# Performance work log

Measured on AMD Instinct MI355X. Metric: run time of the kernel, lower is better.

Reference implementation:

```python
import jax, jax.numpy as jnp
import numpy as np

N_GAUSSIANS = 16
B, D = 32768, 64
LOG_2PI = float(np.log(2.0 * np.pi))


def setup_inputs() -> dict:
    key = jax.random.key(0)
    k1, k2, k3, k4 = jax.random.split(key, 4)
    means = jax.random.normal(k1, (B, N_GAUSSIANS * D), dtype=jnp.float32)
    # strictly positive diagonal variances in [0.5, 1.5)
    covs = jax.random.uniform(k2, (B, N_GAUSSIANS * D), dtype=jnp.float32) + 0.5
    # positive mixture weights (softmax-normalized, like a typical MDN head)
    weights = jax.nn.softmax(jax.random.normal(k3, (B, N_GAUSSIANS), dtype=jnp.float32), axis=-1)
    targets = jax.random.normal(k4, (B, D), dtype=jnp.float32)
    return {"means": means, "covs": covs, "weights": weights, "targets": targets}


def reference(means, covs, weights, targets):
    b = means.shape[0]
    mu = means.reshape(b, N_GAUSSIANS, -1)   # [B, K, D]
    var = covs.reshape(b, N_GAUSSIANS, -1)   # [B, K, D]
    t = targets[:, None, :]                  # [B, 1, D]
    d = mu.shape[-1]
    # analytic diagonal-Gaussian log-prob (same math as MultivariateNormal
    # with diag_embed covariance, without the Cholesky)
    quad = jnp.sum((t - mu) ** 2 / var, axis=-1)          # [B, K]
    logdet = jnp.sum(jnp.log(var), axis=-1)               # [B, K]
    log_probs = -0.5 * (d * LOG_2PI + logdet + quad)      # [B, K]
    log_probs = jnp.clip(log_probs, -100.0, 0.0)
    log_probs_weighted = log_probs + jnp.log(weights)
    total_log_likelihood = jax.nn.logsumexp(log_probs_weighted, axis=1)  # [B]
    return -1.0 * total_log_likelihood
```

## Files before the change

### kernel.cpp

```cpp
#include <hip/hip_runtime.h>
#include <math.h>

#define NG 16
#define DIM 64
#define LOG_2PI 1.8378770664093453f
#define RPW 4
#define WPB 4
#define ROWS_PER_BLOCK (RPW * WPB)

__global__ __launch_bounds__(256) void gmm_loss_kernel(
    const float* __restrict__ means,
    const float* __restrict__ covs,
    const float* __restrict__ weights,
    const float* __restrict__ targets,
    float* __restrict__ out, int B)
{
    const int lane = threadIdx.x & 63;
    const int wave = threadIdx.x >> 6;
    const int g  = lane >> 2;
    const int dq = lane & 3;
    const int fo = lane * 4;

    int b = blockIdx.x * ROWS_PER_BLOCK + wave * RPW;

    #pragma unroll 1
    for (int r = 0; r < RPW; ++r, ++b) {
        if (b >= B) break;

        const float4* m4 = (const float4*)(means + (size_t)b * (NG * DIM)) + fo;
        const float4* v4 = (const float4*)(covs  + (size_t)b * (NG * DIM)) + fo;
        const float4* t4 = (const float4*)(targets + (size_t)b * DIM) + dq * 4;

        const float  w  = weights[(size_t)b * NG + g];
        const float4 m0 = m4[0], m1 = m4[1], m2 = m4[2], m3 = m4[3];
        const float4 v0 = v4[0], v1 = v4[1], v2 = v4[2], v3 = v4[3];
        const float4 t0 = t4[0], t1 = t4[1], t2 = t4[2], t3 = t4[3];

        float p = 0.0f;
        float dx;
        dx = t0.x - m0.x; p += dx * dx * __builtin_amdgcn_rcpf(v0.x);
        dx = t0.y - m0.y; p += dx * dx * __builtin_amdgcn_rcpf(v0.y);
        dx = t0.z - m0.z; p += dx * dx * __builtin_amdgcn_rcpf(v0.z);
        dx = t0.w - m0.w; p += dx * dx * __builtin_amdgcn_rcpf(v0.w);
        p += __logf(v0.x * v0.y * v0.z * v0.w);

        dx = t1.x - m1.x; p += dx * dx * __builtin_amdgcn_rcpf(v1.x);
        dx = t1.y - m1.y; p += dx * dx * __builtin_amdgcn_rcpf(v1.y);
        dx = t1.z - m1.z; p += dx * dx * __builtin_amdgcn_rcpf(v1.z);
        dx = t1.w - m1.w; p += dx * dx * __builtin_amdgcn_rcpf(v1.w);
        p += __logf(v1.x * v1.y * v1.z * v1.w);

        dx = t2.x - m2.x; p += dx * dx * __builtin_amdgcn_rcpf(v2.x);
        dx = t2.y - m2.y; p += dx * dx * __builtin_amdgcn_rcpf(v2.y);
        dx = t2.z - m2.z; p += dx * dx * __builtin_amdgcn_rcpf(v2.z);
        dx = t2.w - m2.w; p += dx * dx * __builtin_amdgcn_rcpf(v2.w);
        p += __logf(v2.x * v2.y * v2.z * v2.w);

        dx = t3.x - m3.x; p += dx * dx * __builtin_amdgcn_rcpf(v3.x);
        dx = t3.y - m3.y; p += dx * dx * __builtin_amdgcn_rcpf(v3.y);
        dx = t3.z - m3.z; p += dx * dx * __builtin_amdgcn_rcpf(v3.z);
        dx = t3.w - m3.w; p += dx * dx * __builtin_amdgcn_rcpf(v3.w);
        p += __logf(v3.x * v3.y * v3.z * v3.w);

        p += __shfl_xor(p, 1);
        p += __shfl_xor(p, 2);

        float lp = -0.5f * (DIM * LOG_2PI + p);
        lp = fminf(fmaxf(lp, -100.0f), 0.0f);
        const float lw = lp + __logf(w);

        float M = lw;
        M = fmaxf(M, __shfl_xor(M, 4));
        M = fmaxf(M, __shfl_xor(M, 8));
        M = fmaxf(M, __shfl_xor(M, 16));
        M = fmaxf(M, __shfl_xor(M, 32));
        float e = __expf(lw - M);
        e += __shfl_xor(e, 4);
        e += __shfl_xor(e, 8);
        e += __shfl_xor(e, 16);
        e += __shfl_xor(e, 32);

        if (lane == 0) out[b] = -(M + __logf(e));
    }
}

extern "C" void kernel_launch(void* const* d_in, const int* in_sizes, int n_in,
                              void* d_out, int out_size, void* d_ws, size_t ws_size,
                              hipStream_t stream) {
    const float* means   = (const float*)d_in[0];
    const float* covs    = (const float*)d_in[1];
    const float* weights = (const float*)d_in[2];
    const float* targets = (const float*)d_in[3];
    float* out = (float*)d_out;

    const int B = in_sizes[0] / (NG * DIM);
    const int grid = (B + ROWS_PER_BLOCK - 1) / ROWS_PER_BLOCK;
    gmm_loss_kernel<<<grid, 256, 0, stream>>>(means, covs, weights, targets, out, B);
}
```

Before: 280.0 us.

## Double-buffer row loads with coalesced nontemporal reads and restructured reductions

Result: faster. 264.6 us (-5.5%).

```diff
diff --git a/kernel.cpp b/kernel.cpp
--- a/kernel.cpp
+++ b/kernel.cpp
@@ -8,6 +8,11 @@
 #define WPB 4
 #define ROWS_PER_BLOCK (RPW * WPB)
 
+typedef float f32x4 __attribute__((ext_vector_type(4)));
+
+
+#define NT(p) __builtin_nontemporal_load(p)
+
 __global__ __launch_bounds__(256) void gmm_loss_kernel(
     const float* __restrict__ means,
     const float* __restrict__ covs,
@@ -17,71 +22,99 @@
 {
     const int lane = threadIdx.x & 63;
     const int wave = threadIdx.x >> 6;
-    const int g  = lane >> 2;
-    const int dq = lane & 3;
-    const int fo = lane * 4;
+    const int G = lane >> 4;
+    const int c = lane & 15;
 
-    int b = blockIdx.x * ROWS_PER_BLOCK + wave * RPW;
+    const int b0 = blockIdx.x * ROWS_PER_BLOCK + wave * RPW;
 
-    #pragma unroll 1
-    for (int r = 0; r < RPW; ++r, ++b) {
-        if (b >= B) break;
+#define ISSUE(S, bb) {                                                        \
+        const int rb = (bb) < B ? (bb) : (B - 1);                             \
+        const f32x4* Mp = (const f32x4*)(means + (size_t)rb * (NG * DIM));    \
+        const f32x4* Vp = (const f32x4*)(covs  + (size_t)rb * (NG * DIM));    \
+        m0##S = NT(Mp + lane);       v0##S = NT(Vp + lane);                   \
+        m1##S = NT(Mp + lane + 64);  v1##S = NT(Vp + lane + 64);              \
+        m2##S = NT(Mp + lane + 128); v2##S = NT(Vp + lane + 128);             \
+        m3##S = NT(Mp + lane + 192); v3##S = NT(Vp + lane + 192);             \
+    }
 
-        const float4* m4 = (const float4*)(means + (size_t)b * (NG * DIM)) + fo;
-        const float4* v4 = (const float4*)(covs  + (size_t)b * (NG * DIM)) + fo;
-        const float4* t4 = (const float4*)(targets + (size_t)b * DIM) + dq * 4;
+#define COMPUTE(S, bb) {                                                      \
+        const int rb = (bb) < B ? (bb) : (B - 1);                             \
+        const f32x4 t = ((const f32x4*)(targets + (size_t)rb * DIM))[c];      \
+        const float* W = weights + (size_t)rb * NG;                           \
+        const float w0 = W[G];     const float w1 = W[G + 4];                 \
+        const float w2 = W[G + 8]; const float w3 = W[G + 12];                \
+        float dx, p0, p1, p2, p3;                                             \
+        dx = t.x - m0##S.x; p0  = dx * dx * __builtin_amdgcn_rcpf(v0##S.x);   \
+        dx = t.y - m0##S.y; p0 += dx * dx * __builtin_amdgcn_rcpf(v0##S.y);   \
+        dx = t.z - m0##S.z; p0 += dx * dx * __builtin_amdgcn_rcpf(v0##S.z);   \
+        dx = t.w - m0##S.w; p0 += dx * dx * __builtin_amdgcn_rcpf(v0##S.w);   \
+        p0 += __logf(v0##S.x * v0##S.y * v0##S.z * v0##S.w);                  \
+        dx = t.x - m1##S.x; p1  = dx * dx * __builtin_amdgcn_rcpf(v1##S.x);   \
+        dx = t.y - m1##S.y; p1 += dx * dx * __builtin_amdgcn_rcpf(v1##S.y);   \
+        dx = t.z - m1##S.z; p1 += dx * dx * __builtin_amdgcn_rcpf(v1##S.z);   \
+        dx = t.w - m1##S.w; p1 += dx * dx * __builtin_amdgcn_rcpf(v1##S.w);   \
+        p1 += __logf(v1##S.x * v1##S.y * v1##S.z * v1##S.w);                  \
+        dx = t.x - m2##S.x; p2  = dx * dx * __builtin_amdgcn_rcpf(v2##S.x);   \
+        dx = t.y - m2##S.y; p2 += dx * dx * __builtin_amdgcn_rcpf(v2##S.y);   \
+        dx = t.z - m2##S.z; p2 += dx * dx * __builtin_amdgcn_rcpf(v2##S.z);   \
+        dx = t.w - m2##S.w; p2 += dx * dx * __builtin_amdgcn_rcpf(v2##S.w);   \
+        p2 += __logf(v2##S.x * v2##S.y * v2##S.z * v2##S.w);                  \
+        dx = t.x - m3##S.x; p3  = dx * dx * __builtin_amdgcn_rcpf(v3##S.x);   \
+        dx = t.y - m3##S.y; p3 += dx * dx * __builtin_amdgcn_rcpf(v3##S.y);   \
+        dx = t.z - m3##S.z; p3 += dx * dx * __builtin_amdgcn_rcpf(v3##S.z);   \
+        dx = t.w - m3##S.w; p3 += dx * dx * __builtin_amdgcn_rcpf(v3##S.w);   \
+        p3 += __logf(v3##S.x * v3##S.y * v3##S.z * v3##S.w);                  \
+        p0 += __shfl_xor(p0, 1); p1 += __shfl_xor(p1, 1);                     \
+        p2 += __shfl_xor(p2, 1); p3 += __shfl_xor(p3, 1);                     \
+        p0 += __shfl_xor(p0, 2); p1 += __shfl_xor(p1, 2);                     \
+        p2 += __shfl_xor(p2, 2); p3 += __shfl_xor(p3, 2);                     \
+        p0 += __shfl_xor(p0, 4); p1 += __shfl_xor(p1, 4);                     \
+        p2 += __shfl_xor(p2, 4); p3 += __shfl_xor(p3, 4);                     \
+        p0 += __shfl_xor(p0, 8); p1 += __shfl_xor(p1, 8);                     \
+        p2 += __shfl_xor(p2, 8); p3 += __shfl_xor(p3, 8);                     \
+        const float base = -0.5f * (DIM * LOG_2PI);                           \
+        float lw0 = base - 0.5f * p0;                                         \
+        float lw1 = base - 0.5f * p1;                                         \
+        float lw2 = base - 0.5f * p2;                                         \
+        float lw3 = base - 0.5f * p3;                                         \
+        lw0 = fminf(fmaxf(lw0, -100.0f), 0.0f) + __logf(w0);                  \
+        lw1 = fminf(fmaxf(lw1, -100.0f), 0.0f) + __logf(w1);                  \
+        lw2 = fminf(fmaxf(lw2, -100.0f), 0.0f) + __logf(w2);                  \
+        lw3 = fminf(fmaxf(lw3, -100.0f), 0.0f) + __logf(w3);                  \
+        float M = fmaxf(fmaxf(lw0, lw1), fmaxf(lw2, lw3));                    \
+        float s = __expf(lw0 - M) + __expf(lw1 - M) +                         \
+                  __expf(lw2 - M) + __expf(lw3 - M);                          \
+        {                                                                     \
+            const float Mo = __shfl_xor(M, 16);                               \
+            const float so = __shfl_xor(s, 16);                               \
+            const float Mn = fmaxf(M, Mo);                                    \
+            s = s * __expf(M - Mn) + so * __expf(Mo - Mn);                    \
+            M = Mn;                                                           \
+        }                                                                     \
+        {                                                                     \
+            const float Mo = __shfl_xor(M, 32);                               \
+            const float so = __shfl_xor(s, 32);                               \
+            const float Mn = fmaxf(M, Mo);                                    \
+            s = s * __expf(M - Mn) + so * __expf(Mo - Mn);                    \
+            M = Mn;                                                           \
+        }                                                                     \
+        if ((bb) < B && lane == 0) out[bb] = -(M + __logf(s));                \
+    }
 
-        const float  w  = weights[(size_t)b * NG + g];
-        const float4 m0 = m4[0], m1 = m4[1], m2 = m4[2], m3 = m4[3];
-        const float4 v0 = v4[0], v1 = v4[1], v2 = v4[2], v3 = v4[3];
-        const float4 t0 = t4[0], t1 = t4[1], t2 = t4[2], t3 = t4[3];
+    f32x4 m0A, m1A, m2A, m3A, v0A, v1A, v2A, v3A;
+    f32x4 m0B, m1B, m2B, m3B, v0B, v1B, v2B, v3B;
 
-        float p = 0.0f;
-        float dx;
-        dx = t0.x - m0.x; p += dx * dx * __builtin_amdgcn_rcpf(v0.x);
-        dx = t0.y - m0.y; p += dx * dx * __builtin_amdgcn_rcpf(v0.y);
-        dx = t0.z - m0.z; p += dx * dx * __builtin_amdgcn_rcpf(v0.z);
-        dx = t0.w - m0.w; p += dx * dx * __builtin_amdgcn_rcpf(v0.w);
-        p += __logf(v0.x * v0.y * v0.z * v0.w);
+    ISSUE(A, b0 + 0)
+    ISSUE(B, b0 + 1)
+    COMPUTE(A, b0 + 0)
+    ISSUE(A, b0 + 2)
+    COMPUTE(B, b0 + 1)
+    ISSUE(B, b0 + 3)
+    COMPUTE(A, b0 + 2)
+    COMPUTE(B, b0 + 3)
 
-        dx = t1.x - m1.x; p += dx * dx * __builtin_amdgcn_rcpf(v1.x);
-        dx = t1.y - m1.y; p += dx * dx * __builtin_amdgcn_rcpf(v1.y);
-        dx = t1.z - m1.z; p += dx * dx * __builtin_amdgcn_rcpf(v1.z);
-        dx = t1.w - m1.w; p += dx * dx * __builtin_amdgcn_rcpf(v1.w);
-        p += __logf(v1.x * v1.y * v1.z * v1.w);
-
-        dx = t2.x - m2.x; p += dx * dx * __builtin_amdgcn_rcpf(v2.x);
-        dx = t2.y - m2.y; p += dx * dx * __builtin_amdgcn_rcpf(v2.y);
-        dx = t2.z - m2.z; p += dx * dx * __builtin_amdgcn_rcpf(v2.z);
-        dx = t2.w - m2.w; p += dx * dx * __builtin_amdgcn_rcpf(v2.w);
-        p += __logf(v2.x * v2.y * v2.z * v2.w);
-
-        dx = t3.x - m3.x; p += dx * dx * __builtin_amdgcn_rcpf(v3.x);
-        dx = t3.y - m3.y; p += dx * dx * __builtin_amdgcn_rcpf(v3.y);
-        dx = t3.z - m3.z; p += dx * dx * __builtin_amdgcn_rcpf(v3.z);
-        dx = t3.w - m3.w; p += dx * dx * __builtin_amdgcn_rcpf(v3.w);
-        p += __logf(v3.x * v3.y * v3.z * v3.w);
-
-        p += __shfl_xor(p, 1);
-        p += __shfl_xor(p, 2);
-
-        float lp = -0.5f * (DIM * LOG_2PI + p);
-        lp = fminf(fmaxf(lp, -100.0f), 0.0f);
-        const float lw = lp + __logf(w);
-
-        float M = lw;
-        M = fmaxf(M, __shfl_xor(M, 4));
-        M = fmaxf(M, __shfl_xor(M, 8));
-        M = fmaxf(M, __shfl_xor(M, 16));
-        M = fmaxf(M, __shfl_xor(M, 32));
-        float e = __expf(lw - M);
-        e += __shfl_xor(e, 4);
-        e += __shfl_xor(e, 8);
-        e += __shfl_xor(e, 16);
-        e += __shfl_xor(e, 32);
-
-        if (lane == 0) out[b] = -(M + __logf(e));
-    }
+#undef ISSUE
+#undef COMPUTE
 }
 
 extern "C" void kernel_launch(void* const* d_in, const int* in_sizes, int n_in,
```
